# Kernel optimization log

Hardware: AMD Instinct MI355X
Metric: run time of the kernel (lower is better)

The kernel has to match this reference:

```python
import jax, jax.numpy as jnp
import numpy as np

HEADS = 4
DIM_HEAD = 64
SCALE = DIM_HEAD ** -0.5
EPS = 1e-5


def setup_inputs() -> dict:
    key = jax.random.key(0)
    k1, k2, k3 = jax.random.split(key, 3)
    b, c, h, w = 16, 256, 64, 64
    hidden = HEADS * DIM_HEAD  # 256
    x = jax.random.normal(k1, (b, c, h, w), dtype=jnp.float32)
    w_qkv = jax.random.normal(k2, (3 * hidden, c), dtype=jnp.float32) * (c ** -0.5)
    w_out = jax.random.normal(k3, (c, hidden), dtype=jnp.float32) * (hidden ** -0.5)
    b_out = jnp.zeros((c,), dtype=jnp.float32)
    g = jnp.ones((c,), dtype=jnp.float32)
    return {"x": x, "w_qkv": w_qkv, "w_out": w_out, "b_out": b_out, "g": g}


def reference(x, w_qkv, w_out, b_out, g):
    b, c, h, w = x.shape
    n = h * w
    hidden = HEADS * DIM_HEAD
    # 1x1 conv to qkv: [b, 3*hidden, h, w]
    qkv = jnp.einsum('oc,bcxy->boxy', w_qkv, x)
    qkv = qkv.reshape(b, 3, HEADS, DIM_HEAD, n)  # split q/k/v and heads
    q, k, v = qkv[:, 0], qkv[:, 1], qkv[:, 2]    # each [b, H, d, n]
    q = jax.nn.softmax(q, axis=-2)               # softmax over feature dim d
    k = jax.nn.softmax(k, axis=-1)               # softmax over token dim n
    v = v / n
    q = q * SCALE
    context = jnp.einsum('bhdn,bhen->bhde', k, v)  # [b,H,d,e]
    out = jnp.einsum('bhde,bhdn->bhen', context, q)  # [b,H,e,n]
    out = out.reshape(b, hidden, h, w)
    # to_out: 1x1 conv + channel LayerNorm with scale g
    y = jnp.einsum('oc,bcxy->boxy', w_out, out) + b_out[None, :, None, None]
    mean = jnp.mean(y, axis=1, keepdims=True)
    var = jnp.var(y, axis=1, keepdims=True)
    return (y - mean) * jax.lax.rsqrt(var + EPS) * g[None, :, None, None]
```

## Files before the change

kernel.cpp:

```cpp
#include <hip/hip_runtime.h>
#include <cstddef>
#include <cstdint>

#define NHEADS 4
#define DHEAD 64
#define CIN 256
#define HID 256
#define MQKV 768
#define NPIX 4096
#define NBATCH 16
#define ATT_SCALE 0.125f
#define LN_EPS 1e-5f

typedef float f32x4 __attribute__((ext_vector_type(4)));
typedef short s16x8 __attribute__((ext_vector_type(8)));
typedef unsigned short ushort;

static constexpr size_t OFF_QKV  = 0;
static constexpr size_t OFF_KSUM = (size_t)NBATCH * MQKV * NPIX;
static constexpr size_t OFF_CTX  = OFF_KSUM + 4096;
static constexpr size_t OFF_WA   = OFF_CTX + 262144;
static constexpr size_t OFF_WH   = OFF_WA + 1048576;
static constexpr size_t OFF_WL   = OFF_WH + 98304;

__device__ __forceinline__ unsigned pack_bf(float v) {
  unsigned u = __float_as_uint(v);
  unsigned hi = (u + 0x7fffu + ((u >> 16) & 1u)) >> 16;
  float fh = __uint_as_float(hi << 16);
  float rr = v - fh;
  unsigned u2 = __float_as_uint(rr);
  unsigned lo = (u2 + 0x7fffu + ((u2 >> 16) & 1u)) >> 16;
  return (hi << 16) | (lo & 0xffffu);
}

__device__ __forceinline__ void gload_lds16(const void* gsrc, void* ldst) {
  __builtin_amdgcn_global_load_lds(
      (const __attribute__((address_space(1))) unsigned int*)gsrc,
      (__attribute__((address_space(3))) unsigned int*)ldst, 16, 0, 0);
}

__global__ __launch_bounds__(256) void k_wsplit(const float* __restrict__ W,
                                                ushort* __restrict__ WH,
                                                ushort* __restrict__ WL) {
  const int pid = blockIdx.x * 256 + threadIdx.x;
  const int m = pid >> 5, pp = pid & 31;
  const int wdw = pp >> 2, p = pp & 3;
  const int sp = p ^ ((m >> 1) & 3);
  const float* src = W + (size_t)m * 256 + wdw * 32 + sp * 8;
  s16x8 hv, lv;
#pragma unroll
  for (int e = 0; e < 8; ++e) {
    unsigned pk = pack_bf(src[e]);
    hv[e] = (short)(pk >> 16);
    lv[e] = (short)(pk & 0xffffu);
  }
  *(s16x8*)&WH[(size_t)m * 256 + pp * 8] = hv;
  *(s16x8*)&WL[(size_t)m * 256 + pp * 8] = lv;
}

__global__ __launch_bounds__(256, 2) void k_qkv_mfma(const ushort* __restrict__ WH,
                                                     const ushort* __restrict__ WL,
                                                     const float* __restrict__ X,
                                                     float* __restrict__ Y) {
  __shared__ ushort AHs[2][4096];
  __shared__ ushort ALs[2][4096];
  __shared__ unsigned int BTs[2][4096];

  const int t = threadIdx.x;
  const int lane = t & 63;
  const int w = t >> 6;
  const int wy = w >> 1, wx = w & 1;
  const int m0 = blockIdx.x * 128;
  const int n0 = blockIdx.y * 128;
  const int b  = blockIdx.z;
  const float* Xb = X + (size_t)b * CIN * NPIX;
  float* Yb = Y + (size_t)b * MQKV * NPIX;

  const int r = lane & 15, g = lane >> 4;
  const int bn0 = (t & 31) * 4;
  const int bcq = t >> 5;
  const int bc0 = bcq * 4;

  f32x4 acc[4][4];
#pragma unroll
  for (int i = 0; i < 4; ++i)
#pragma unroll
    for (int j = 0; j < 4; ++j) acc[i][j] = (f32x4){0.f, 0.f, 0.f, 0.f};

  float4 bx[4];

  {
#pragma unroll
    for (int ch = 0; ch < 2; ++ch) {
      const int slot = ch * 256 + t;
      const int row = slot >> 2, pc = slot & 3;
      gload_lds16(WH + (size_t)(m0 + row) * 256 + pc * 8, &AHs[0][slot * 8]);
      gload_lds16(WL + (size_t)(m0 + row) * 256 + pc * 8, &ALs[0][slot * 8]);
    }
#pragma unroll
    for (int i = 0; i < 4; ++i)
      bx[i] = *(const float4*)&Xb[(size_t)(bc0 + i) * NPIX + n0 + bn0];
    unsigned pk[4][4];
#pragma unroll
    for (int i = 0; i < 4; ++i) {
      pk[0][i] = pack_bf(bx[i].x); pk[1][i] = pack_bf(bx[i].y);
      pk[2][i] = pack_bf(bx[i].z); pk[3][i] = pack_bf(bx[i].w);
    }
#pragma unroll
    for (int j = 0; j < 4; ++j) {
      const int nl = bn0 + j;
      const int s = bcq ^ (nl & 7);
      uint4 q4; q4.x = pk[j][0]; q4.y = pk[j][1]; q4.z = pk[j][2]; q4.w = pk[j][3];
      *(uint4*)&BTs[0][nl * 32 + s * 4] = q4;
    }
  }
  __syncthreads();

  for (int kc = 0; kc < 8; ++kc) {
    const int cur = kc & 1;
    const int nxt = cur ^ 1;
    if (kc < 7) {
#pragma unroll
      for (int ch = 0; ch < 2; ++ch) {
        const int slot = ch * 256 + t;
        const int row = slot >> 2, pc = slot & 3;
        gload_lds16(WH + (size_t)(m0 + row) * 256 + (kc + 1) * 32 + pc * 8, &AHs[nxt][slot * 8]);
        gload_lds16(WL + (size_t)(m0 + row) * 256 + (kc + 1) * 32 + pc * 8, &ALs[nxt][slot * 8]);
      }
#pragma unroll
      for (int i = 0; i < 4; ++i)
        bx[i] = *(const float4*)&Xb[(size_t)((kc + 1) * 32 + bc0 + i) * NPIX + n0 + bn0];
    }

    s16x8 ah[4], al[4], bh[4], bl[4];
#pragma unroll
    for (int mt = 0; mt < 4; ++mt) {
      const int mr = wy * 64 + mt * 16 + r;
      const int p = g ^ ((mr >> 1) & 3);
      ah[mt] = *(const s16x8*)&AHs[cur][mr * 32 + p * 8];
      al[mt] = *(const s16x8*)&ALs[cur][mr * 32 + p * 8];
    }
#pragma unroll
    for (int nt = 0; nt < 4; ++nt) {
      const int nl = wx * 64 + nt * 16 + r;
      const int s0 = (2 * g) ^ (nl & 7);
      const int s1 = (2 * g + 1) ^ (nl & 7);
      const uint4 u0 = *(const uint4*)&BTs[cur][nl * 32 + s0 * 4];
      const uint4 u1 = *(const uint4*)&BTs[cur][nl * 32 + s1 * 4];
      s16x8 hv, lv;
      hv[0] = (short)(u0.x >> 16); lv[0] = (short)u0.x;
      hv[1] = (short)(u0.y >> 16); lv[1] = (short)u0.y;
      hv[2] = (short)(u0.z >> 16); lv[2] = (short)u0.z;
      hv[3] = (short)(u0.w >> 16); lv[3] = (short)u0.w;
      hv[4] = (short)(u1.x >> 16); lv[4] = (short)u1.x;
      hv[5] = (short)(u1.y >> 16); lv[5] = (short)u1.y;
      hv[6] = (short)(u1.z >> 16); lv[6] = (short)u1.z;
      hv[7] = (short)(u1.w >> 16); lv[7] = (short)u1.w;
      bh[nt] = hv; bl[nt] = lv;
    }

#pragma unroll
    for (int mt = 0; mt < 4; ++mt)
#pragma unroll
      for (int nt = 0; nt < 4; ++nt) {
        acc[mt][nt] = __builtin_amdgcn_mfma_f32_16x16x32_bf16(ah[mt], bh[nt], acc[mt][nt], 0, 0, 0);
        acc[mt][nt] = __builtin_amdgcn_mfma_f32_16x16x32_bf16(ah[mt], bl[nt], acc[mt][nt], 0, 0, 0);
        acc[mt][nt] = __builtin_amdgcn_mfma_f32_16x16x32_bf16(al[mt], bh[nt], acc[mt][nt], 0, 0, 0);
      }

    if (kc < 7) {
      unsigned pk[4][4];
#pragma unroll
      for (int i = 0; i < 4; ++i) {
        pk[0][i] = pack_bf(bx[i].x); pk[1][i] = pack_bf(bx[i].y);
        pk[2][i] = pack_bf(bx[i].z); pk[3][i] = pack_bf(bx[i].w);
      }
#pragma unroll
      for (int j = 0; j < 4; ++j) {
        const int nl = bn0 + j;
        const int s = bcq ^ (nl & 7);
        uint4 q4; q4.x = pk[j][0]; q4.y = pk[j][1]; q4.z = pk[j][2]; q4.w = pk[j][3];
        *(uint4*)&BTs[nxt][nl * 32 + s * 4] = q4;
      }
    }
    __syncthreads();
  }

#pragma unroll
  for (int mt = 0; mt < 4; ++mt) {
    const int mrow = m0 + wy * 64 + mt * 16 + g * 4;
#pragma unroll
    for (int nt = 0; nt < 4; ++nt) {
      const int ncol = n0 + wx * 64 + nt * 16 + r;
#pragma unroll
      for (int j = 0; j < 4; ++j)
        Yb[(size_t)(mrow + j) * NPIX + ncol] = acc[mt][nt][j];
    }
  }
}

__global__ __launch_bounds__(256) void k_context(const float* __restrict__ QKV,
                                                 float* __restrict__ CTX,
                                                 float* __restrict__ KSUM) {
  const int bh = blockIdx.x;
  const int chunk = blockIdx.y;
  const int b = bh >> 2, h = bh & 3;
  const float* Kb = QKV + ((size_t)b * MQKV + HID + h * DHEAD) * NPIX;
  const float* Vb = QKV + ((size_t)b * MQKV + 2 * HID + h * DHEAD) * NPIX;
  const int t = threadIdx.x;

  __shared__ float ekT[64][68];
  __shared__ float vT[64][68];

  const int ld = t >> 2;
  const int lf = t & 3;
  const int dr = t >> 4;
  const int er = t & 15;

  float acc[4][4] = {{0.f}};
  float ssum = 0.f;

  for (int sub = 0; sub < 4; ++sub) {
    const int n0 = chunk * 256 + sub * 64;
#pragma unroll
    for (int i = 0; i < 4; ++i) {
      const int c = lf * 4 + i * 16;
      float4 kv = *(const float4*)&Kb[(size_t)ld * NPIX + n0 + c];
      float4 vv = *(const float4*)&Vb[(size_t)ld * NPIX + n0 + c];
      const float e0 = __expf(kv.x), e1 = __expf(kv.y), e2 = __expf(kv.z), e3 = __expf(kv.w);
      ekT[c + 0][ld] = e0; ekT[c + 1][ld] = e1;
      ekT[c + 2][ld] = e2; ekT[c + 3][ld] = e3;
      ssum += e0 + e1 + e2 + e3;
      vT[c + 0][ld] = vv.x; vT[c + 1][ld] = vv.y;
      vT[c + 2][ld] = vv.z; vT[c + 3][ld] = vv.w;
    }
    __syncthreads();
#pragma unroll 8
    for (int nn = 0; nn < 64; ++nn) {
      const float4 a = *(const float4*)&ekT[nn][dr * 4];
      const float4 bb = *(const float4*)&vT[nn][er * 4];
      const float ra[4] = {a.x, a.y, a.z, a.w};
      const float rb[4] = {bb.x, bb.y, bb.z, bb.w};
#pragma unroll
      for (int i = 0; i < 4; ++i)
#pragma unroll
        for (int j = 0; j < 4; ++j) acc[i][j] = fmaf(ra[i], rb[j], acc[i][j]);
    }
    __syncthreads();
  }
  ssum += __shfl_xor(ssum, 1);
  ssum += __shfl_xor(ssum, 2);
  if ((t & 3) == 0) atomicAdd(&KSUM[bh * 64 + ld], ssum);

#pragma unroll
  for (int i = 0; i < 4; ++i)
#pragma unroll
    for (int j = 0; j < 4; ++j)
      atomicAdd(&CTX[((size_t)bh * 64 + dr * 4 + i) * 64 + er * 4 + j], acc[i][j]);
}

__global__ __launch_bounds__(256) void k_wct2(const float* __restrict__ Wout,
                                              const float* __restrict__ CTX,
                                              const float* __restrict__ KSUMp,
                                              unsigned* __restrict__ WA) {
  const int h = blockIdx.x, b = blockIdx.y;
  const int bh = b * 4 + h;
  const int o = threadIdx.x;
  const float* Cb = CTX + (size_t)bh * 4096;
  const float* Kb = KSUMp + bh * 64;

  float wv[64];
#pragma unroll
  for (int i = 0; i < 16; ++i) {
    float4 w4 = *(const float4*)&Wout[(size_t)o * HID + h * DHEAD + i * 4];
    wv[i * 4 + 0] = w4.x; wv[i * 4 + 1] = w4.y;
    wv[i * 4 + 2] = w4.z; wv[i * 4 + 3] = w4.w;
  }
  unsigned* WAb = WA + (size_t)b * 65536;
  for (int dg = 0; dg < 16; ++dg) {
    float s[4];
#pragma unroll
    for (int j = 0; j < 4; ++j) {
      const int d = dg * 4 + j;
      float a0 = 0, a1 = 0;
#pragma unroll
      for (int e = 0; e < 64; e += 2) {
        a0 = fmaf(wv[e], Cb[d * 64 + e], a0);
        a1 = fmaf(wv[e + 1], Cb[d * 64 + e + 1], a1);
      }
      s[j] = a0 + a1;
    }
    const float4 ks = *(const float4*)&Kb[dg * 4];
    uint4 q4;
    q4.x = pack_bf(s[0] * (ATT_SCALE / (4096.0f * ks.x)));
    q4.y = pack_bf(s[1] * (ATT_SCALE / (4096.0f * ks.y)));
    q4.z = pack_bf(s[2] * (ATT_SCALE / (4096.0f * ks.z)));
    q4.w = pack_bf(s[3] * (ATT_SCALE / (4096.0f * ks.w)));
    const int wnd = h * 2 + (dg >> 3);
    const int slot = (dg & 7) ^ (o & 7);
    *(uint4*)&WAb[(size_t)wnd * 8192 + o * 32 + slot * 4] = q4;
  }
}

__global__ __launch_bounds__(512, 1) void k_final2(const float* __restrict__ QKV,
                                                   const unsigned* __restrict__ WA,
                                                   const float* __restrict__ bout,
                                                   const float* __restrict__ gin,
                                                   float* __restrict__ OUT) {
  __shared__ __align__(16) unsigned char Ubuf[65536];
  __shared__ __align__(16) unsigned AS[2][8192];
  __shared__ float rs[4][64];
  __shared__ float csum[64], csq[64];
  __shared__ float bo_s[256], g_s[256];
  float* QF = (float*)Ubuf;
  unsigned* QT = (unsigned*)Ubuf;

  const int t = threadIdx.x;
  const int lane = t & 63;
  const int w = t >> 6;
  const int wm = w >> 1, wn = w & 1;
  const int r = lane & 15, gq = lane >> 4;
  const int b = blockIdx.y;
  const int n0 = blockIdx.x * 64;

  if (t < 64) { csum[t] = 0.f; csq[t] = 0.f; }
  if (t < 256) bo_s[t] = bout[t];
  else g_s[t - 256] = gin[t - 256];

  const float* Qsrc = QKV + (size_t)b * MQKV * NPIX + n0;
  const unsigned* WAb = WA + (size_t)b * 65536;

#pragma unroll
  for (int i = 0; i < 8; ++i) {
    const int s = i * 512 + t;
    const int row = s >> 4, c16 = s & 15;
    gload_lds16(Qsrc + (size_t)row * NPIX + c16 * 4, (char*)QF + (size_t)s * 16);
  }
  __syncthreads();

  if (w < 4) {
    const int col = lane, h = w;
    float ssum = 0.f;
#pragma unroll
    for (int d = 0; d < 64; ++d) {
      const float e = __expf(QF[(h * 64 + d) * 64 + col]);
      QF[(h * 64 + d) * 64 + col] = e;
      ssum += e;
    }
    rs[h][col] = 1.0f / ssum;
  } else {
#pragma unroll
    for (int q = 0; q < 8; ++q) {
      const int s = q * 256 + (t - 256);
      gload_lds16(WAb + s * 4, (char*)&AS[0][0] + s * 16);
    }
  }
  __syncthreads();

  {
    const int col = t & 63, w8 = t >> 6;
    const float rscale = rs[w8 >> 1][col];
    unsigned pkv[32];
#pragma unroll
    for (int i = 0; i < 32; ++i)
      pkv[i] = pack_bf(QF[(w8 * 32 + i) * 64 + col] * rscale);
    __syncthreads();
#pragma unroll
    for (int p = 0; p < 8; ++p) {
      uint4 q4;
      q4.x = pkv[p * 4 + 0]; q4.y = pkv[p * 4 + 1];
      q4.z = pkv[p * 4 + 2]; q4.w = pkv[p * 4 + 3];
      *(uint4*)&QT[col * 256 + w8 * 32 + ((p ^ (col & 7)) * 4)] = q4;
    }
  }
  __syncthreads();

  f32x4 acc[4][2];
#pragma unroll
  for (int i = 0; i < 4; ++i)
#pragma unroll
    for (int j = 0; j < 2; ++j) acc[i][j] = (f32x4){0.f, 0.f, 0.f, 0.f};

  for (int kc = 0; kc < 8; ++kc) {
    const int cur = kc & 1, nxt = cur ^ 1;
    if (kc < 7) {
#pragma unroll
      for (int q = 0; q < 4; ++q) {
        const int s = q * 512 + t;
        gload_lds16(WAb + (kc + 1) * 8192 + s * 4, (char*)&AS[nxt][0] + s * 16);
      }
    }
    s16x8 ah[4], al[4], bh[2], bl[2];
#pragma unroll
    for (int mt = 0; mt < 4; ++mt) {
      const int o = wm * 64 + mt * 16 + r;
      const uint4 u0 = *(const uint4*)&AS[cur][o * 32 + (((2 * gq) ^ (r & 7)) * 4)];
      const uint4 u1 = *(const uint4*)&AS[cur][o * 32 + (((2 * gq + 1) ^ (r & 7)) * 4)];
      s16x8 hv, lv;
      hv[0] = (short)(u0.x >> 16); lv[0] = (short)u0.x;
      hv[1] = (short)(u0.y >> 16); lv[1] = (short)u0.y;
      hv[2] = (short)(u0.z >> 16); lv[2] = (short)u0.z;
      hv[3] = (short)(u0.w >> 16); lv[3] = (short)u0.w;
      hv[4] = (short)(u1.x >> 16); lv[4] = (short)u1.x;
      hv[5] = (short)(u1.y >> 16); lv[5] = (short)u1.y;
      hv[6] = (short)(u1.z >> 16); lv[6] = (short)u1.z;
      hv[7] = (short)(u1.w >> 16); lv[7] = (short)u1.w;
      ah[mt] = hv; al[mt] = lv;
    }
#pragma unroll
    for (int nt = 0; nt < 2; ++nt) {
      const int col = wn * 32 + nt * 16 + r;
      const uint4 u0 = *(const uint4*)&QT[col * 256 + kc * 32 + (((2 * gq) ^ (r & 7)) * 4)];
      const uint4 u1 = *(const uint4*)&QT[col * 256 + kc * 32 + (((2 * gq + 1) ^ (r & 7)) * 4)];
      s16x8 hv, lv;
      hv[0] = (short)(u0.x >> 16); lv[0] = (short)u0.x;
      hv[1] = (short)(u0.y >> 16); lv[1] = (short)u0.y;
      hv[2] = (short)(u0.z >> 16); lv[2] = (short)u0.z;
      hv[3] = (short)(u0.w >> 16); lv[3] = (short)u0.w;
      hv[4] = (short)(u1.x >> 16); lv[4] = (short)u1.x;
      hv[5] = (short)(u1.y >> 16); lv[5] = (short)u1.y;
      hv[6] = (short)(u1.z >> 16); lv[6] = (short)u1.z;
      hv[7] = (short)(u1.w >> 16); lv[7] = (short)u1.w;
      bh[nt] = hv; bl[nt] = lv;
    }
#pragma unroll
    for (int mt = 0; mt < 4; ++mt)
#pragma unroll
      for (int nt = 0; nt < 2; ++nt) {
        acc[mt][nt] = __builtin_amdgcn_mfma_f32_16x16x32_bf16(ah[mt], bh[nt], acc[mt][nt], 0, 0, 0);
        acc[mt][nt] = __builtin_amdgcn_mfma_f32_16x16x32_bf16(ah[mt], bl[nt], acc[mt][nt], 0, 0, 0);
        acc[mt][nt] = __builtin_amdgcn_mfma_f32_16x16x32_bf16(al[mt], bh[nt], acc[mt][nt], 0, 0, 0);
      }
    __syncthreads();
  }

  float psum[2] = {0.f, 0.f}, psq[2] = {0.f, 0.f};
#pragma unroll
  for (int mt = 0; mt < 4; ++mt)
#pragma unroll
    for (int nt = 0; nt < 2; ++nt)
#pragma unroll
      for (int j = 0; j < 4; ++j) {
        const int o = wm * 64 + mt * 16 + gq * 4 + j;
        const float y = acc[mt][nt][j] + bo_s[o];
        acc[mt][nt][j] = y;
        psum[nt] += y;
        psq[nt] += y * y;
      }
#pragma unroll
  for (int nt = 0; nt < 2; ++nt) {
    const int col = wn * 32 + nt * 16 + r;
    atomicAdd(&csum[col], psum[nt]);
    atomicAdd(&csq[col], psq[nt]);
  }
  __syncthreads();
  float mean[2], rstd[2];
#pragma unroll
  for (int nt = 0; nt < 2; ++nt) {
    const int col = wn * 32 + nt * 16 + r;
    const float m = csum[col] * (1.0f / 256.0f);
    const float v = csq[col] * (1.0f / 256.0f) - m * m;
    mean[nt] = m;
    rstd[nt] = rsqrtf(v + LN_EPS);
  }
#pragma unroll
  for (int mt = 0; mt < 4; ++mt)
#pragma unroll
    for (int j = 0; j < 4; ++j) {
      const int o = wm * 64 + mt * 16 + gq * 4 + j;
      const float gm = g_s[o];
#pragma unroll
      for (int nt = 0; nt < 2; ++nt) {
        const int col = wn * 32 + nt * 16 + r;
        OUT[((size_t)b * HID + o) * NPIX + n0 + col] =
            (acc[mt][nt][j] - mean[nt]) * rstd[nt] * gm;
      }
    }
}

extern "C" void kernel_launch(void* const* d_in, const int* in_sizes, int n_in,
                              void* d_out, int out_size, void* d_ws, size_t ws_size,
                              hipStream_t stream) {
  const float* x     = (const float*)d_in[0];
  const float* w_qkv = (const float*)d_in[1];
  const float* w_out = (const float*)d_in[2];
  const float* b_out = (const float*)d_in[3];
  const float* g     = (const float*)d_in[4];
  float* out = (float*)d_out;
  float* ws = (float*)d_ws;

  float* QKV  = ws + OFF_QKV;
  float* KSUM = ws + OFF_KSUM;
  float* CTX  = ws + OFF_CTX;
  unsigned* WA = (unsigned*)(ws + OFF_WA);
  ushort* WH  = (ushort*)(ws + OFF_WH);
  ushort* WL  = (ushort*)(ws + OFF_WL);

  hipMemsetAsync(KSUM, 0, (4096 + 262144) * sizeof(float), stream);
  k_wsplit<<<96, 256, 0, stream>>>(w_qkv, WH, WL);
  k_qkv_mfma<<<dim3(6, 32, 16), 256, 0, stream>>>(WH, WL, x, QKV);
  k_context<<<dim3(64, 16), 256, 0, stream>>>(QKV, CTX, KSUM);
  k_wct2<<<dim3(4, 16), 256, 0, stream>>>(w_out, CTX, KSUM, WA);
  k_final2<<<dim3(64, 16), 512, 0, stream>>>(QKV, WA, b_out, g, out);
}
```

Measured before the change: 440.4 us.

## Use split-bf16 MFMA for context, XCD-aware QKV tile order, new LDS swizzle

The context reduction k^T v now runs on MFMA with hi/lo bf16 splitting, reading K and V straight from global memory into registers. This replaces the FP32 FMA loop that staged tiles through LDS, and halves the number of chunk blocks. The QKV GEMM grid is flattened and remapped so that the six M-tiles sharing one X tile land on the same XCD, which should improve L2 reuse. Its B-tile LDS swizzle also changes to reduce bank conflicts. The 3-term bf16 split keeps accuracy close to fp32 but drops the lo×lo term. The context loads are strided per lane, which may be less coalesced.

```diff
diff --git a/kernel.cpp b/kernel.cpp
--- a/kernel.cpp
+++ b/kernel.cpp
@@ -39,6 +39,8 @@
       (__attribute__((address_space(3))) unsigned int*)ldst, 16, 0, 0);
 }
 
+#define BSWZ(nl) ((((nl) & 7) ^ (((nl) >> 2) & 7)) & 7)
+
 __global__ __launch_bounds__(256) void k_wsplit(const float* __restrict__ W,
                                                 ushort* __restrict__ WH,
                                                 ushort* __restrict__ WL) {
@@ -70,9 +72,17 @@
   const int lane = t & 63;
   const int w = t >> 6;
   const int wy = w >> 1, wx = w & 1;
-  const int m0 = blockIdx.x * 128;
-  const int n0 = blockIdx.y * 128;
-  const int b  = blockIdx.z;
+
+  const int D = blockIdx.x;
+  const int xcd = D & 7;
+  const int jj = D >> 3;
+  const int mtile = jj % 6;
+  const int gi = jj / 6;
+  const int grp = xcd + (gi << 3);
+  const int m0 = mtile * 128;
+  const int n0 = (grp & 31) * 128;
+  const int b  = grp >> 5;
+
   const float* Xb = X + (size_t)b * CIN * NPIX;
   float* Yb = Y + (size_t)b * MQKV * NPIX;
 
@@ -109,7 +119,7 @@
 #pragma unroll
     for (int j = 0; j < 4; ++j) {
       const int nl = bn0 + j;
-      const int s = bcq ^ (nl & 7);
+      const int s = bcq ^ BSWZ(nl);
       uint4 q4; q4.x = pk[j][0]; q4.y = pk[j][1]; q4.z = pk[j][2]; q4.w = pk[j][3];
       *(uint4*)&BTs[0][nl * 32 + s * 4] = q4;
     }
@@ -143,8 +153,8 @@
 #pragma unroll
     for (int nt = 0; nt < 4; ++nt) {
       const int nl = wx * 64 + nt * 16 + r;
-      const int s0 = (2 * g) ^ (nl & 7);
-      const int s1 = (2 * g + 1) ^ (nl & 7);
+      const int s0 = (2 * g) ^ BSWZ(nl);
+      const int s1 = (2 * g + 1) ^ BSWZ(nl);
       const uint4 u0 = *(const uint4*)&BTs[cur][nl * 32 + s0 * 4];
       const uint4 u1 = *(const uint4*)&BTs[cur][nl * 32 + s1 * 4];
       s16x8 hv, lv;
@@ -178,7 +188,7 @@
 #pragma unroll
       for (int j = 0; j < 4; ++j) {
         const int nl = bn0 + j;
-        const int s = bcq ^ (nl & 7);
+        const int s = bcq ^ BSWZ(nl);
         uint4 q4; q4.x = pk[j][0]; q4.y = pk[j][1]; q4.z = pk[j][2]; q4.w = pk[j][3];
         *(uint4*)&BTs[nxt][nl * 32 + s * 4] = q4;
       }
@@ -199,64 +209,93 @@
   }
 }
 
-__global__ __launch_bounds__(256) void k_context(const float* __restrict__ QKV,
-                                                 float* __restrict__ CTX,
-                                                 float* __restrict__ KSUM) {
+__global__ __launch_bounds__(256) void k_context3(const float* __restrict__ QKV,
+                                                  float* __restrict__ CTX,
+                                                  float* __restrict__ KSUM) {
   const int bh = blockIdx.x;
   const int chunk = blockIdx.y;
   const int b = bh >> 2, h = bh & 3;
   const float* Kb = QKV + ((size_t)b * MQKV + HID + h * DHEAD) * NPIX;
   const float* Vb = QKV + ((size_t)b * MQKV + 2 * HID + h * DHEAD) * NPIX;
   const int t = threadIdx.x;
-
-  __shared__ float ekT[64][68];
-  __shared__ float vT[64][68];
-
-  const int ld = t >> 2;
-  const int lf = t & 3;
-  const int dr = t >> 4;
-  const int er = t & 15;
-
-  float acc[4][4] = {{0.f}};
-  float ssum = 0.f;
-
-  for (int sub = 0; sub < 4; ++sub) {
-    const int n0 = chunk * 256 + sub * 64;
-#pragma unroll
-    for (int i = 0; i < 4; ++i) {
-      const int c = lf * 4 + i * 16;
-      float4 kv = *(const float4*)&Kb[(size_t)ld * NPIX + n0 + c];
-      float4 vv = *(const float4*)&Vb[(size_t)ld * NPIX + n0 + c];
-      const float e0 = __expf(kv.x), e1 = __expf(kv.y), e2 = __expf(kv.z), e3 = __expf(kv.w);
-      ekT[c + 0][ld] = e0; ekT[c + 1][ld] = e1;
-      ekT[c + 2][ld] = e2; ekT[c + 3][ld] = e3;
-      ssum += e0 + e1 + e2 + e3;
-      vT[c + 0][ld] = vv.x; vT[c + 1][ld] = vv.y;
-      vT[c + 2][ld] = vv.z; vT[c + 3][ld] = vv.w;
-    }
-    __syncthreads();
-#pragma unroll 8
-    for (int nn = 0; nn < 64; ++nn) {
-      const float4 a = *(const float4*)&ekT[nn][dr * 4];
-      const float4 bb = *(const float4*)&vT[nn][er * 4];
-      const float ra[4] = {a.x, a.y, a.z, a.w};
-      const float rb[4] = {bb.x, bb.y, bb.z, bb.w};
-#pragma unroll
-      for (int i = 0; i < 4; ++i)
-#pragma unroll
-        for (int j = 0; j < 4; ++j) acc[i][j] = fmaf(ra[i], rb[j], acc[i][j]);
-    }
-    __syncthreads();
-  }
-  ssum += __shfl_xor(ssum, 1);
-  ssum += __shfl_xor(ssum, 2);
-  if ((t & 3) == 0) atomicAdd(&KSUM[bh * 64 + ld], ssum);
-
-#pragma unroll
-  for (int i = 0; i < 4; ++i)
-#pragma unroll
-    for (int j = 0; j < 4; ++j)
-      atomicAdd(&CTX[((size_t)bh * 64 + dr * 4 + i) * 64 + er * 4 + j], acc[i][j]);
+  const int lane = t & 63, w = t >> 6;
+  const int wy = w >> 1, wx = w & 1;
+  const int r = lane & 15, gq = lane >> 4;
+
+  f32x4 acc[2][2];
+#pragma unroll
+  for (int i = 0; i < 2; ++i)
+#pragma unroll
+    for (int j = 0; j < 2; ++j) acc[i][j] = (f32x4){0.f, 0.f, 0.f, 0.f};
+  float ksums[2] = {0.f, 0.f};
+
+  const int nb = chunk * 512 + gq * 8;
+
+  for (int step = 0; step < 16; ++step) {
+    const int n0 = nb + step * 32;
+    s16x8 ah2[2], al2[2], bh2[2], bl2[2];
+#pragma unroll
+    for (int mt = 0; mt < 2; ++mt) {
+      const int d = wy * 32 + mt * 16 + r;
+      const float4 x0 = *(const float4*)&Kb[(size_t)d * NPIX + n0];
+      const float4 x1 = *(const float4*)&Kb[(size_t)d * NPIX + n0 + 4];
+      float ev[8];
+      ev[0] = __expf(x0.x); ev[1] = __expf(x0.y);
+      ev[2] = __expf(x0.z); ev[3] = __expf(x0.w);
+      ev[4] = __expf(x1.x); ev[5] = __expf(x1.y);
+      ev[6] = __expf(x1.z); ev[7] = __expf(x1.w);
+      s16x8 hv, lv;
+#pragma unroll
+      for (int i = 0; i < 8; ++i) {
+        const unsigned pk = pack_bf(ev[i]);
+        hv[i] = (short)(pk >> 16); lv[i] = (short)(pk & 0xffffu);
+        ksums[mt] += ev[i];
+      }
+      ah2[mt] = hv; al2[mt] = lv;
+    }
+#pragma unroll
+    for (int nt = 0; nt < 2; ++nt) {
+      const int e = wx * 32 + nt * 16 + r;
+      const float4 x0 = *(const float4*)&Vb[(size_t)e * NPIX + n0];
+      const float4 x1 = *(const float4*)&Vb[(size_t)e * NPIX + n0 + 4];
+      const float vv[8] = {x0.x, x0.y, x0.z, x0.w, x1.x, x1.y, x1.z, x1.w};
+      s16x8 hv, lv;
+#pragma unroll
+      for (int i = 0; i < 8; ++i) {
+        const unsigned pk = pack_bf(vv[i]);
+        hv[i] = (short)(pk >> 16); lv[i] = (short)(pk & 0xffffu);
+      }
+      bh2[nt] = hv; bl2[nt] = lv;
+    }
+#pragma unroll
+    for (int mt = 0; mt < 2; ++mt)
+#pragma unroll
+      for (int nt = 0; nt < 2; ++nt) {
+        acc[mt][nt] = __builtin_amdgcn_mfma_f32_16x16x32_bf16(ah2[mt], bh2[nt], acc[mt][nt], 0, 0, 0);
+        acc[mt][nt] = __builtin_amdgcn_mfma_f32_16x16x32_bf16(ah2[mt], bl2[nt], acc[mt][nt], 0, 0, 0);
+        acc[mt][nt] = __builtin_amdgcn_mfma_f32_16x16x32_bf16(al2[mt], bh2[nt], acc[mt][nt], 0, 0, 0);
+      }
+  }
+
+#pragma unroll
+  for (int mt = 0; mt < 2; ++mt) {
+    float ss = ksums[mt];
+    ss += __shfl_xor(ss, 16);
+    ss += __shfl_xor(ss, 32);
+    if (wx == 0 && gq == 0)
+      atomicAdd(&KSUM[bh * 64 + wy * 32 + mt * 16 + r], ss);
+  }
+
+#pragma unroll
+  for (int mt = 0; mt < 2; ++mt)
+#pragma unroll
+    for (int nt = 0; nt < 2; ++nt)
+#pragma unroll
+      for (int j = 0; j < 4; ++j) {
+        const int d = wy * 32 + mt * 16 + gq * 4 + j;
+        const int e = wx * 32 + nt * 16 + r;
+        atomicAdd(&CTX[((size_t)bh * 64 + d) * 64 + e], acc[mt][nt][j]);
+      }
 }
 
 __global__ __launch_bounds__(256) void k_wct2(const float* __restrict__ Wout,
@@ -498,8 +537,8 @@
 
   hipMemsetAsync(KSUM, 0, (4096 + 262144) * sizeof(float), stream);
   k_wsplit<<<96, 256, 0, stream>>>(w_qkv, WH, WL);
-  k_qkv_mfma<<<dim3(6, 32, 16), 256, 0, stream>>>(WH, WL, x, QKV);
-  k_context<<<dim3(64, 16), 256, 0, stream>>>(QKV, CTX, KSUM);
+  k_qkv_mfma<<<dim3(3072), 256, 0, stream>>>(WH, WL, x, QKV);
+  k_context3<<<dim3(64, 8), 256, 0, stream>>>(QKV, CTX, KSUM);
   k_wct2<<<dim3(4, 16), 256, 0, stream>>>(w_out, CTX, KSUM, WA);
   k_final2<<<dim3(64, 16), 512, 0, stream>>>(QKV, WA, b_out, g, out);
 }
```

After: 398.4 us. 9.5% less time.
